# Kernel tuning notes

Measured on AMD Instinct MI355X. Metric: run time of the kernel, lower is better.

## Reference

```python
import jax, jax.numpy as jnp
import numpy as np

OMEGA_0 = 30.0  # SIREN frequency from config.kernel.omega_0


def setup_inputs() -> dict:
    key = jax.random.key(0)
    ks = jax.random.split(key, 8)
    B, Ci, Co, L, H = 8, 64, 64, 8192, 32
    x = jax.random.normal(ks[0], (B, Ci, L), dtype=jnp.float32)
    # SIREN-style kernel-net params (Linear(1,H) -> sin -> Linear(H,H) -> sin -> Linear(H, Co*Ci))
    w1 = jax.random.uniform(ks[1], (1, H), jnp.float32, -1.0, 1.0)
    b1 = jax.random.uniform(ks[2], (H,), jnp.float32, -1.0, 1.0)
    c = np.sqrt(6.0 / H) / OMEGA_0
    w2 = jax.random.uniform(ks[3], (H, H), jnp.float32, -c, c)
    b2 = jax.random.uniform(ks[4], (H,), jnp.float32, -c, c)
    w3 = jax.random.uniform(ks[5], (H, Co * Ci), jnp.float32, -c, c)
    b3 = jax.random.uniform(ks[6], (Co * Ci,), jnp.float32, -c, c)
    bias = jnp.zeros((Co,), dtype=jnp.float32)  # CKConv bias init: fill_(0.0)
    return {"x": x, "w1": w1, "b1": b1, "w2": w2, "b2": b2,
            "w3": w3, "b3": b3, "bias": bias}


def reference(x, w1, b1, w2, b2, w3, b3, bias):
    B, Ci, L = x.shape
    Co = bias.shape[0]
    # 1. relative positions in [-1, 1], one per input sample
    rel = jnp.linspace(-1.0, 1.0, L).astype(x.dtype)[:, None]        # (L, 1)
    # 2. SIREN kernel net -> continuous kernel sampled at L positions
    h = jnp.sin(OMEGA_0 * (rel @ w1 + b1))                            # (L, H)
    h = jnp.sin(OMEGA_0 * (h @ w2 + b2))                              # (L, H)
    k = (h @ w3 + b3)                                                 # (L, Co*Ci)
    kernel = k.T.reshape(Co, Ci, L)                                   # (Co, Ci, L)
    # 3. causal full-length conv1d. torch's causal_padding (left zero-pad of
    #    x by K-1, plus a left zero on an even-length kernel) + conv1d
    #    (cross-correlation) is mathematically y[t] = sum_{tau<=t} x[t-tau] *
    #    kernel_flipped[tau], i.e. a causal linear convolution with the
    #    time-reversed kernel. Computed exactly via zero-padded FFT (N=2L >=
    #    L+L-1, so no circular wraparound) instead of O(L^2) direct conv.
    kr = kernel[:, :, ::-1]                                           # flip time axis
    N = 2 * L
    Xf = jnp.fft.rfft(x, n=N, axis=-1)                                # (B, Ci, N/2+1)
    Kf = jnp.fft.rfft(kr, n=N, axis=-1)                               # (Co, Ci, N/2+1)
    Yf = jnp.einsum('bif,oif->bof', Xf, Kf)                           # contract in-channels
    y = jnp.fft.irfft(Yf, n=N, axis=-1)[:, :, :L]                     # (B, Co, L)
    return y + bias[None, :, None]
```

## Files before the change

### kernel.cpp

```cpp
#include <hip/hip_runtime.h>


#define LSEQ   8192
#define N2     8192
#define HDIM   32
#define NB     33
#define NROWS  512
#define NFREQ  8193
#define FSTRIDE 8200
#define FBLK   8
#define FTH    1024
#define OMEGA0 30.0f
#define TWOPI  6.283185307179586f

#define IDX(i) ((i) + ((i) >> 4))

__global__ __launch_bounds__(256) void prep_basis_kernel(
    const float* __restrict__ w1, const float* __restrict__ b1,
    const float* __restrict__ w2, const float* __restrict__ b2,
    float* __restrict__ hbT)
{
    int t = blockIdx.x * 256 + threadIdx.x;
    float rel = -1.0f + 2.0f * (float)t / (float)(LSEQ - 1);
    float h1[HDIM];
    #pragma unroll
    for (int j = 0; j < HDIM; ++j)
        h1[j] = sinf(OMEGA0 * fmaf(rel, w1[j], b1[j]));
    for (int j = 0; j < HDIM; ++j) {
        float acc = b2[j];
        #pragma unroll 8
        for (int j2 = 0; j2 < HDIM; ++j2)
            acc = fmaf(h1[j2], w2[j2 * HDIM + j], acc);
        hbT[j * LSEQ + (LSEQ - 1 - t)] = sinf(OMEGA0 * acc);
    }
    hbT[HDIM * LSEQ + t] = 1.0f;
}

__global__ __launch_bounds__(256) void prep_m2_kernel(
    const float* __restrict__ w3, const float* __restrict__ b3,
    float* __restrict__ M2)
{
    int idx = blockIdx.x * 256 + threadIdx.x;
    if (idx >= NB * 64 * 64) return;
    int o = idx & 63;
    int i = (idx >> 6) & 63;
    int r = idx >> 12;
    M2[idx] = (r < HDIM) ? w3[r * 4096 + o * 64 + i] : b3[o * 64 + i];
}

__device__ __forceinline__ float2 tw8k(const float2* Tq, int t)
{
    bool mir = t > 1024;
    int u = mir ? 2048 - t : t;
    float2 e = Tq[u];
    float c = mir ? e.y : e.x;
    float s = mir ? e.x : e.y;
    return make_float2(c, -s);
}

__device__ __forceinline__ void build_table(float2* Tq, int tid)
{
    for (int t = tid; t <= 1024; t += FTH) {
        float s, c;
        __sincosf(TWOPI * (float)t / 8192.0f, &s, &c);
        Tq[t] = make_float2(c, s);
    }
}

__device__ __forceinline__ void fft8192_core(float* re, float* im,
                                             const float2* Tq, int tid)
{
    for (int p = 11; p >= 1; p -= 2) {
        int m = 1 << p;
        int lmul = 11 - p;
        __syncthreads();
        for (int u = tid; u < 2048; u += FTH) {
            int j = u & (m - 1);
            int base = ((u >> p) << (p + 2)) + j;
            int i0 = IDX(base), i1 = IDX(base + m), i2 = IDX(base + 2 * m), i3 = IDX(base + 3 * m);
            float ar = re[i0], ai = im[i0];
            float br = re[i1], bi = im[i1];
            float cr = re[i2], ci = im[i2];
            float dr = re[i3], di = im[i3];
            float t0r = ar + cr, t0i = ai + ci;
            float t1r = ar - cr, t1i = ai - ci;
            float t2r = br + dr, t2i = bi + di;
            float t3r = br - dr, t3i = bi - di;
            float q0r = t0r + t2r, q0i = t0i + t2i;
            float q2r = t0r - t2r, q2i = t0i - t2i;
            float q1r = t1r + t3i, q1i = t1i - t3r;
            float q3r = t1r - t3i, q3i = t1i + t3r;
            float2 w1 = tw8k(Tq, j << lmul);
            float w2r = w1.x * w1.x - w1.y * w1.y;
            float w2i = 2.0f * w1.x * w1.y;
            float w3r = w2r * w1.x - w2i * w1.y;
            float w3i = w2r * w1.y + w2i * w1.x;
            re[i0] = q0r;                     im[i0] = q0i;
            re[i1] = q2r * w2r - q2i * w2i;   im[i1] = q2r * w2i + q2i * w2r;
            re[i2] = q1r * w1.x - q1i * w1.y; im[i2] = q1r * w1.y + q1i * w1.x;
            re[i3] = q3r * w3r - q3i * w3i;   im[i3] = q3r * w3i + q3i * w3r;
        }
    }
    __syncthreads();
    for (int u = tid; u < 4096; u += FTH) {
        int a = IDX(2 * u), b = IDX(2 * u + 1);
        float ar = re[a], ai = im[a];
        float br = re[b], bi = im[b];
        re[a] = ar + br; im[a] = ai + bi;
        re[b] = ar - br; im[b] = ai - bi;
    }
    __syncthreads();
    for (int idx = tid; idx < N2; idx += FTH) {
        unsigned r = __brev((unsigned)idx) >> 19;
        if ((int)r > idx) {
            int pa = IDX(idx), pb = IDX((int)r);
            float tr = re[pa], ti = im[pa];
            re[pa] = re[pb]; im[pa] = im[pb];
            re[pb] = tr;     im[pb] = ti;
        }
    }
    __syncthreads();
}

__global__ __launch_bounds__(FTH) void rfft_rows_kernel(
    const float* __restrict__ in, float* __restrict__ outF)
{
    __shared__ float re[8704], im[8704];
    __shared__ float2 Tq[1025];
    int tid = threadIdx.x;
    int row = blockIdx.x;

    build_table(Tq, tid);

    const float2* zin = (const float2*)(in + (long long)row * LSEQ);
    for (int n = tid; n < 4096; n += FTH) {
        float2 v = zin[n];
        re[IDX(n)] = v.x;            im[IDX(n)] = v.y;
        re[IDX(n + 4096)] = 0.0f;    im[IDX(n + 4096)] = 0.0f;
    }
    fft8192_core(re, im, Tq, tid);

    float2* out = (float2*)outF + (long long)row * FSTRIDE;
    for (int k = tid; k <= 8192; k += FTH) {
        int k1 = IDX(k & (N2 - 1));
        int k2 = IDX((N2 - k) & (N2 - 1));
        float zr = re[k1], zi = im[k1];
        float wr = re[k2], wi = im[k2];
        float er = 0.5f * (zr + wr), ei = 0.5f * (zi - wi);
        float pr = 0.5f * (zi + wi), pi = 0.5f * (wr - zr);
        float s, c;
        __sincosf(-TWOPI * (float)k / 16384.0f, &s, &c);
        out[k] = make_float2(er + c * pr - s * pi,
                             ei + c * pi + s * pr);
    }
}

__global__ __launch_bounds__(512, 8) void contract_kernel(
    const float* __restrict__ Hf, const float* __restrict__ M2,
    float* __restrict__ XYf)
{
    __shared__ float2 Ks[FBLK][8][64];
    __shared__ __align__(16) float2 Xq[8][8][FBLK];
    int tid = threadIdx.x;
    int o = tid & 63;
    int w = tid >> 6;
    long long f0 = (long long)blockIdx.x * FBLK;

    const float* Hblk = Hf + (size_t)blockIdx.x * (FBLK * 2);

    float2 yacc[FBLK];
    #pragma unroll
    for (int f = 0; f < FBLK; ++f) yacc[f] = make_float2(0.f, 0.f);

    int sf  = tid & 7;
    int sii = (tid >> 3) & 7;
    int sb  = tid >> 6;

    for (int oct = 0; oct < 8; ++oct) {
        __syncthreads();

        const float2* xsrc = (const float2*)XYf
            + (long long)((sb << 6) + (oct << 3) + sii) * FSTRIDE + f0 + sf;
        float2 xstage = *xsrc;

        float2 kacc[FBLK];
        #pragma unroll
        for (int f = 0; f < FBLK; ++f) kacc[f] = make_float2(0.f, 0.f);

        const float* mp = M2 + (((oct << 3) + w) << 6) + o;
        #pragma unroll 3
        for (int r = 0; r < NB; ++r) {
            const float4* hp = (const float4*)(Hblk + (size_t)r * (size_t)(FSTRIDE * 2));
            float4 h0 = hp[0], h1 = hp[1], h2 = hp[2], h3 = hp[3];
            float m0 = mp[r << 12];
            float hr_[FBLK] = {h0.x,h0.z,h1.x,h1.z,h2.x,h2.z,h3.x,h3.z};
            float hi_[FBLK] = {h0.y,h0.w,h1.y,h1.w,h2.y,h2.w,h3.y,h3.w};
            #pragma unroll
            for (int f = 0; f < FBLK; ++f) {
                kacc[f].x = fmaf(m0, hr_[f], kacc[f].x);
                kacc[f].y = fmaf(m0, hi_[f], kacc[f].y);
            }
        }
        Xq[sb][sii][sf] = xstage;
        #pragma unroll
        for (int f = 0; f < FBLK; ++f)
            Ks[f][w][o] = kacc[f];
        __syncthreads();

        #pragma unroll 2
        for (int ii = 0; ii < 8; ++ii) {
            const float4* xp = (const float4*)(&Xq[w][ii][0]);
            float4 x0 = xp[0], x1 = xp[1], x2 = xp[2], x3 = xp[3];
            float xr[FBLK] = {x0.x,x0.z,x1.x,x1.z,x2.x,x2.z,x3.x,x3.z};
            float xi[FBLK] = {x0.y,x0.w,x1.y,x1.w,x2.y,x2.w,x3.y,x3.w};
            #pragma unroll
            for (int f = 0; f < FBLK; ++f) {
                float2 kv = Ks[f][ii][o];
                yacc[f].x = fmaf(xr[f], kv.x, fmaf(-xi[f], kv.y, yacc[f].x));
                yacc[f].y = fmaf(xr[f], kv.y, fmaf( xi[f], kv.x, yacc[f].y));
            }
        }
    }
    __syncthreads();

    long long row = (long long)((w << 6) + o);
    float2* yp = (float2*)XYf + row * FSTRIDE + f0;
    #pragma unroll
    for (int f = 0; f < FBLK; ++f)
        if (f0 + f < NFREQ) yp[f] = yacc[f];
}

__global__ __launch_bounds__(FTH) void irfft_rows_kernel(
    const float* __restrict__ Yf, const float* __restrict__ bias,
    float* __restrict__ out)
{
    __shared__ float re[8704], im[8704];
    __shared__ float2 Tq[1025];
    int tid = threadIdx.x;
    int row = blockIdx.x;
    int o = row & 63;

    build_table(Tq, tid);

    const float2* G = (const float2*)Yf + (long long)row * FSTRIDE;
    for (int k = tid; k < N2; k += FTH) {
        float2 gk = G[k];
        float2 gm = G[8192 - k];
        float er = 0.5f * (gk.x + gm.x), ei = 0.5f * (gk.y - gm.y);
        float pr = 0.5f * (gk.x - gm.x), pi = 0.5f * (gk.y + gm.y);
        float s, c;
        __sincosf(TWOPI * (float)k / 16384.0f, &s, &c);
        float or_ = pr * c - pi * s;
        float oi_ = pr * s + pi * c;
        re[IDX(k)] = er - oi_;
        im[IDX(k)] = -(ei + or_);
    }
    fft8192_core(re, im, Tq, tid);

    float bo = bias[o];
    const float scale = 1.0f / 8192.0f;
    float2* op = (float2*)(out + (long long)row * LSEQ);
    for (int n = tid; n < 4096; n += FTH) {
        int pn = IDX(n);
        op[n] = make_float2(fmaf(re[pn], scale, bo), fmaf(-im[pn], scale, bo));
    }
}

extern "C" void kernel_launch(void* const* d_in, const int* in_sizes, int n_in,
                              void* d_out, int out_size, void* d_ws, size_t ws_size,
                              hipStream_t stream)
{
    const float* x    = (const float*)d_in[0];
    const float* w1   = (const float*)d_in[1];
    const float* b1   = (const float*)d_in[2];
    const float* w2   = (const float*)d_in[3];
    const float* b2   = (const float*)d_in[4];
    const float* w3   = (const float*)d_in[5];
    const float* b3   = (const float*)d_in[6];
    const float* bias = (const float*)d_in[7];
    float* out = (float*)d_out;

    float* ws  = (float*)d_ws;
    float* hbT = ws;
    float* Hf  = hbT + NB * LSEQ;
    float* M2  = Hf + NB * FSTRIDE * 2;
    float* XYf = M2 + NB * 64 * 64;

    prep_basis_kernel<<<dim3(LSEQ / 256), dim3(256), 0, stream>>>(w1, b1, w2, b2, hbT);
    prep_m2_kernel<<<dim3((NB * 64 * 64 + 255) / 256), dim3(256), 0, stream>>>(w3, b3, M2);
    rfft_rows_kernel<<<dim3(NB), dim3(FTH), 0, stream>>>(hbT, Hf);
    rfft_rows_kernel<<<dim3(NROWS), dim3(FTH), 0, stream>>>(x, XYf);
    contract_kernel<<<dim3((NFREQ + FBLK - 1) / FBLK), dim3(512), 0, stream>>>(Hf, M2, XYf);
    irfft_rows_kernel<<<dim3(NROWS), dim3(FTH), 0, stream>>>(XYf, bias, out);
}
```

Measured before the change: 258.6 us.

## Remap contract threads to frequency-per-thread and preload kernel-net weights into registers

In the contraction stage each thread now owns one frequency and accumulates across all 8 batches, instead of owning one batch and accumulating across 8 frequencies. Each thread reads a single kernel value per in-channel from shared memory and broadcast-reads the X values. The 33 M2 weights per thread are loaded into registers ahead of the basis-accumulation loop, and the occupancy hint drops from 8 to 6 waves. The aim is fewer shared-memory loads per FMA and better latency hiding for the M2 loads, at the cost of more registers and output stores that are strided across rows.

```diff
diff --git a/kernel.cpp b/kernel.cpp
--- a/kernel.cpp
+++ b/kernel.cpp
@@ -155,7 +155,7 @@
     }
 }
 
-__global__ __launch_bounds__(512, 8) void contract_kernel(
+__global__ __launch_bounds__(512, 6) void contract_kernel(
     const float* __restrict__ Hf, const float* __restrict__ M2,
     float* __restrict__ XYf)
 {
@@ -168,9 +168,9 @@
 
     const float* Hblk = Hf + (size_t)blockIdx.x * (FBLK * 2);
 
-    float2 yacc[FBLK];
+    float2 yacc[8];
     #pragma unroll
-    for (int f = 0; f < FBLK; ++f) yacc[f] = make_float2(0.f, 0.f);
+    for (int b = 0; b < 8; ++b) yacc[b] = make_float2(0.f, 0.f);
 
     int sf  = tid & 7;
     int sii = (tid >> 3) & 7;
@@ -183,22 +183,25 @@
             + (long long)((sb << 6) + (oct << 3) + sii) * FSTRIDE + f0 + sf;
         float2 xstage = *xsrc;
 
+        const float* mp = M2 + (((oct << 3) + w) << 6) + o;
+        float m[NB];
+        #pragma unroll
+        for (int r = 0; r < NB; ++r) m[r] = mp[r << 12];
+
         float2 kacc[FBLK];
         #pragma unroll
         for (int f = 0; f < FBLK; ++f) kacc[f] = make_float2(0.f, 0.f);
 
-        const float* mp = M2 + (((oct << 3) + w) << 6) + o;
         #pragma unroll 3
         for (int r = 0; r < NB; ++r) {
             const float4* hp = (const float4*)(Hblk + (size_t)r * (size_t)(FSTRIDE * 2));
             float4 h0 = hp[0], h1 = hp[1], h2 = hp[2], h3 = hp[3];
-            float m0 = mp[r << 12];
             float hr_[FBLK] = {h0.x,h0.z,h1.x,h1.z,h2.x,h2.z,h3.x,h3.z};
             float hi_[FBLK] = {h0.y,h0.w,h1.y,h1.w,h2.y,h2.w,h3.y,h3.w};
             #pragma unroll
             for (int f = 0; f < FBLK; ++f) {
-                kacc[f].x = fmaf(m0, hr_[f], kacc[f].x);
-                kacc[f].y = fmaf(m0, hi_[f], kacc[f].y);
+                kacc[f].x = fmaf(m[r], hr_[f], kacc[f].x);
+                kacc[f].y = fmaf(m[r], hi_[f], kacc[f].y);
             }
         }
         Xq[sb][sii][sf] = xstage;
@@ -209,25 +212,24 @@
 
         #pragma unroll 2
         for (int ii = 0; ii < 8; ++ii) {
-            const float4* xp = (const float4*)(&Xq[w][ii][0]);
-            float4 x0 = xp[0], x1 = xp[1], x2 = xp[2], x3 = xp[3];
-            float xr[FBLK] = {x0.x,x0.z,x1.x,x1.z,x2.x,x2.z,x3.x,x3.z};
-            float xi[FBLK] = {x0.y,x0.w,x1.y,x1.w,x2.y,x2.w,x3.y,x3.w};
+            float2 kv = Ks[w][ii][o];
             #pragma unroll
-            for (int f = 0; f < FBLK; ++f) {
-                float2 kv = Ks[f][ii][o];
-                yacc[f].x = fmaf(xr[f], kv.x, fmaf(-xi[f], kv.y, yacc[f].x));
-                yacc[f].y = fmaf(xr[f], kv.y, fmaf( xi[f], kv.x, yacc[f].y));
+            for (int b = 0; b < 8; ++b) {
+                float2 xv = Xq[b][ii][w];
+                yacc[b].x = fmaf(xv.x, kv.x, fmaf(-xv.y, kv.y, yacc[b].x));
+                yacc[b].y = fmaf(xv.x, kv.y, fmaf( xv.y, kv.x, yacc[b].y));
             }
         }
     }
     __syncthreads();
 
-    long long row = (long long)((w << 6) + o);
-    float2* yp = (float2*)XYf + row * FSTRIDE + f0;
-    #pragma unroll
-    for (int f = 0; f < FBLK; ++f)
-        if (f0 + f < NFREQ) yp[f] = yacc[f];
+    if (f0 + w < NFREQ) {
+        #pragma unroll
+        for (int b = 0; b < 8; ++b) {
+            long long row = (long long)((b << 6) + o);
+            ((float2*)XYf)[row * FSTRIDE + f0 + w] = yacc[b];
+        }
+    }
 }
 
 __global__ __launch_bounds__(FTH) void irfft_rows_kernel(
```

After: 347.9 us. 34.5% more time.

## Fuse basis generation, M2 packing and both forward FFTs into one launch

Applied to the files above, without the earlier changes.

Replaces the four launches (basis prep, M2 pack, basis rfft, input rfft) with a single fwd_kernel whose blocks are partitioned by role. Basis rows are now computed directly in shared memory inside the FFT block instead of going through a global hbT buffer, and the M2 packing runs as extra blocks in the same grid. The aim is to remove launch overhead and a global round trip. In exchange, each basis thread recomputes all 32 first-layer sines per row (32x redundant sin work), and those 32 basis blocks may become a tail inside the larger grid.

```diff
diff --git a/kernel.cpp b/kernel.cpp
--- a/kernel.cpp
+++ b/kernel.cpp
@@ -14,39 +14,6 @@
 #define TWOPI  6.283185307179586f
 
 #define IDX(i) ((i) + ((i) >> 4))
-
-__global__ __launch_bounds__(256) void prep_basis_kernel(
-    const float* __restrict__ w1, const float* __restrict__ b1,
-    const float* __restrict__ w2, const float* __restrict__ b2,
-    float* __restrict__ hbT)
-{
-    int t = blockIdx.x * 256 + threadIdx.x;
-    float rel = -1.0f + 2.0f * (float)t / (float)(LSEQ - 1);
-    float h1[HDIM];
-    #pragma unroll
-    for (int j = 0; j < HDIM; ++j)
-        h1[j] = sinf(OMEGA0 * fmaf(rel, w1[j], b1[j]));
-    for (int j = 0; j < HDIM; ++j) {
-        float acc = b2[j];
-        #pragma unroll 8
-        for (int j2 = 0; j2 < HDIM; ++j2)
-            acc = fmaf(h1[j2], w2[j2 * HDIM + j], acc);
-        hbT[j * LSEQ + (LSEQ - 1 - t)] = sinf(OMEGA0 * acc);
-    }
-    hbT[HDIM * LSEQ + t] = 1.0f;
-}
-
-__global__ __launch_bounds__(256) void prep_m2_kernel(
-    const float* __restrict__ w3, const float* __restrict__ b3,
-    float* __restrict__ M2)
-{
-    int idx = blockIdx.x * 256 + threadIdx.x;
-    if (idx >= NB * 64 * 64) return;
-    int o = idx & 63;
-    int i = (idx >> 6) & 63;
-    int r = idx >> 12;
-    M2[idx] = (r < HDIM) ? w3[r * 4096 + o * 64 + i] : b3[o * 64 + i];
-}
 
 __device__ __forceinline__ float2 tw8k(const float2* Tq, int t)
 {
@@ -122,25 +89,70 @@
     __syncthreads();
 }
 
-__global__ __launch_bounds__(FTH) void rfft_rows_kernel(
-    const float* __restrict__ in, float* __restrict__ outF)
-{
+__global__ __launch_bounds__(FTH) void fwd_kernel(
+    const float* __restrict__ x,
+    const float* __restrict__ w1, const float* __restrict__ b1,
+    const float* __restrict__ w2, const float* __restrict__ b2,
+    const float* __restrict__ w3, const float* __restrict__ b3,
+    float* __restrict__ Hf, float* __restrict__ XYf, float* __restrict__ M2)
+{
+    int blk = blockIdx.x;
+    int tid = threadIdx.x;
+
+    if (blk >= NB + NROWS) {
+        int idx = (blk - (NB + NROWS)) * FTH + tid;
+        if (idx < NB * 64 * 64) {
+            int o = idx & 63;
+            int i = (idx >> 6) & 63;
+            int r = idx >> 12;
+            M2[idx] = (r < HDIM) ? w3[r * 4096 + o * 64 + i] : b3[o * 64 + i];
+        }
+        return;
+    }
+
     __shared__ float re[8704], im[8704];
     __shared__ float2 Tq[1025];
-    int tid = threadIdx.x;
-    int row = blockIdx.x;
-
     build_table(Tq, tid);
 
-    const float2* zin = (const float2*)(in + (long long)row * LSEQ);
-    for (int n = tid; n < 4096; n += FTH) {
-        float2 v = zin[n];
-        re[IDX(n)] = v.x;            im[IDX(n)] = v.y;
-        re[IDX(n + 4096)] = 0.0f;    im[IDX(n + 4096)] = 0.0f;
-    }
+    float* outF;
+    long long orow;
+    if (blk < NB) {
+        int r = blk;
+        for (int n = tid; n < 4096; n += FTH) {
+            re[IDX(n + 4096)] = 0.0f;  im[IDX(n + 4096)] = 0.0f;
+        }
+        if (r < HDIM) {
+            for (int t = tid; t < LSEQ; t += FTH) {
+                float rel = -1.0f + 2.0f * (float)t / (float)(LSEQ - 1);
+                float acc = b2[r];
+                #pragma unroll 8
+                for (int j = 0; j < HDIM; ++j)
+                    acc = fmaf(sinf(OMEGA0 * fmaf(rel, w1[j], b1[j])), w2[j * HDIM + r], acc);
+                float g = sinf(OMEGA0 * acc);
+                int s = LSEQ - 1 - t;
+                if (s & 1) im[IDX(s >> 1)] = g;
+                else       re[IDX(s >> 1)] = g;
+            }
+        } else {
+            for (int n = tid; n < 4096; n += FTH) {
+                re[IDX(n)] = 1.0f;  im[IDX(n)] = 1.0f;
+            }
+        }
+        outF = Hf;  orow = r;
+    } else {
+        int row = blk - NB;
+        const float2* zin = (const float2*)(x + (long long)row * LSEQ);
+        for (int n = tid; n < 4096; n += FTH) {
+            float2 v = zin[n];
+            re[IDX(n)] = v.x;            im[IDX(n)] = v.y;
+            re[IDX(n + 4096)] = 0.0f;    im[IDX(n + 4096)] = 0.0f;
+        }
+        outF = XYf;  orow = row;
+    }
+
     fft8192_core(re, im, Tq, tid);
 
-    float2* out = (float2*)outF + (long long)row * FSTRIDE;
+    float2* out = (float2*)outF + orow * FSTRIDE;
     for (int k = tid; k <= 8192; k += FTH) {
         int k1 = IDX(k & (N2 - 1));
         int k2 = IDX((N2 - k) & (N2 - 1));
@@ -286,10 +298,9 @@
     float* M2  = Hf + NB * FSTRIDE * 2;
     float* XYf = M2 + NB * 64 * 64;
 
-    prep_basis_kernel<<<dim3(LSEQ / 256), dim3(256), 0, stream>>>(w1, b1, w2, b2, hbT);
-    prep_m2_kernel<<<dim3((NB * 64 * 64 + 255) / 256), dim3(256), 0, stream>>>(w3, b3, M2);
-    rfft_rows_kernel<<<dim3(NB), dim3(FTH), 0, stream>>>(hbT, Hf);
-    rfft_rows_kernel<<<dim3(NROWS), dim3(FTH), 0, stream>>>(x, XYf);
+    int m2blocks = (NB * 64 * 64 + FTH - 1) / FTH;
+    fwd_kernel<<<dim3(NB + NROWS + m2blocks), dim3(FTH), 0, stream>>>(
+        x, w1, b1, w2, b2, w3, b3, Hf, XYf, M2);
     contract_kernel<<<dim3((NFREQ + FBLK - 1) / FBLK), dim3(512), 0, stream>>>(Hf, M2, XYf);
     irfft_rows_kernel<<<dim3(NROWS), dim3(FTH), 0, stream>>>(XYf, bias, out);
 }
```

New measurement: 243.6 us. -5.8%, faster.
